# Optimization experiments

Hardware: AMD Instinct MI355X
Metric: run time of the kernel (lower is better)

Reference implementation:

```python
import jax, jax.numpy as jnp
import numpy as np

N_ITEMS = 50001   # n_items + 1 (padding row 0)
DIM = 256         # item_embedding_dim == hidden_size
PURPOSES = 3
TAU = 0.1
SEQ_LEN = 50
BATCH = 128
EPS = 0.01
STDV = 1.0 / np.sqrt(DIM)


def setup_inputs() -> dict:
    key = jax.random.key(0)
    ks = jax.random.split(key, 7)
    u = lambda k, s: jax.random.uniform(k, s, jnp.float32, -STDV, STDV)
    emb = u(ks[0], (N_ITEMS, DIM)).at[0].set(0.0)  # padding_idx=0
    emb_purpose = u(ks[1], (PURPOSES, DIM))
    w_ih = u(ks[2], (PURPOSES, 3 * DIM, DIM))
    w_hh = u(ks[3], (PURPOSES, 3 * DIM, DIM))
    b_ih = u(ks[4], (PURPOSES, 3 * DIM))
    b_hh = u(ks[5], (PURPOSES, 3 * DIM))
    seq = jax.random.randint(ks[6], (SEQ_LEN, BATCH), 0, N_ITEMS)
    return {"seq": seq, "emb": emb, "emb_purpose": emb_purpose,
            "w_ih": w_ih, "w_hh": w_hh, "b_ih": b_ih, "b_hh": b_hh}


def _psru(w_ih, w_hh, b_ih, b_hh, seq_embs, concen):
    # seq_embs: [B,S,D], concen: [B,S] -> final hidden [B,D]
    B = seq_embs.shape[0]
    H = w_hh.shape[1]

    def cell(h, xs):
        x, c = xs  # x: [B,D], c: [B]
        gi = x @ w_ih.T + b_ih
        gh = h @ w_hh.T + b_hh
        i_r, i_i, i_n = jnp.split(gi, 3, axis=1)
        h_r, h_i, h_n = jnp.split(gh, 3, axis=1)
        resetgate = jax.nn.sigmoid(i_r + h_r)
        inputgate = jax.nn.sigmoid(i_i + h_i)
        newgate = jnp.tanh(i_n + resetgate * h_n)
        cf = jnp.where(c >= EPS, c, 0.0)[:, None]  # concen gating
        hy = h - cf * inputgate * (h - newgate)
        return hy, None

    h0 = jnp.zeros((B, H), seq_embs.dtype)
    hN, _ = jax.lax.scan(cell, h0, (jnp.swapaxes(seq_embs, 0, 1), concen.T))
    return hN


def reference(seq, emb, emb_purpose, w_ih, w_hh, b_ih, b_hh):
    s = seq.T                               # [B,S]
    mask = (s != 0).astype(emb.dtype)       # padding mask
    seq_embs = emb[s]                       # [B,S,D]
    concen_score = jnp.einsum('bsd,pd->bsp', seq_embs, emb_purpose)
    concen_w = jax.nn.softmax(concen_score / TAU, axis=2) * mask[:, :, None]
    # run one PSRU per purpose, batched with vmap over the purpose axis
    hn = jax.vmap(_psru, in_axes=(0, 0, 0, 0, None, 2))(
        w_ih, w_hh, b_ih, b_hh, seq_embs, concen_w)   # [P,B,D]
    # target = arange(n_items) -> pos_embs = full embedding table
    tcw = jax.nn.softmax(emb @ emb_purpose.T, axis=1)  # [T,P]
    # scores[b,t] = sum_p tcw[t,p] * <hn[p,b,:], emb[t,:]>
    scores = jnp.einsum('pbd,td,tp->bt', hn, emb, tcw)  # [B,T]
    return scores
```

## Files before the change

kernel.cpp:

```cpp
#include <hip/hip_runtime.h>
#include <hip/hip_bf16.h>

#define S_LEN 50
#define BATCH 128
#define DIM 256
#define NITEMS 50001
#define NPAD 50048
#define GDIM 768
#define NSEQ 6400

typedef __attribute__((ext_vector_type(8))) short short8;
typedef __attribute__((ext_vector_type(4))) short short4_;
typedef __attribute__((ext_vector_type(4))) float float4_;

static __device__ __forceinline__ unsigned short f2bf(float x){
  union { float f; unsigned u; } v; v.f = x;
  unsigned r = v.u + 0x7FFFu + ((v.u >> 16) & 1u);
  return (unsigned short)(r >> 16);
}
static __device__ __forceinline__ float bf2f(unsigned short h){
  union { unsigned u; float f; } v; v.u = ((unsigned)h) << 16;
  return v.f;
}
static __device__ __forceinline__ float rcpf_(float x){ return __builtin_amdgcn_rcpf(x); }
static __device__ __forceinline__ float exp2f_(float x){ return __builtin_amdgcn_exp2f(x); }

__global__ __launch_bounds__(256) void k_prep(
        const float* __restrict__ wih, const float* __restrict__ whh,
        unsigned short* __restrict__ wihT, unsigned short* __restrict__ whh_bf,
        const float* __restrict__ emb, const float* __restrict__ embp,
        unsigned short* __restrict__ embT, float* __restrict__ tcw,
        const int* __restrict__ seq, unsigned short* __restrict__ xT,
        float* __restrict__ cfb){
  __shared__ unsigned short sT[8192];
  int bid = blockIdx.x;
  int tid = threadIdx.x;
  if (bid < 576){
    int i = bid*256 + tid;
    float4_ y = ((const float4_*)whh)[i];
    short4_ v;
    #pragma unroll
    for (int j=0;j<4;j++) v[j] = (short)f2bf(y[j]);
    ((short4_*)whh_bf)[i] = v;
    return;
  }
  int w = tid >> 6, lane = tid & 63;
  int r16 = w*4 + (lane >> 4);
  int c0  = lane & 15;
  if (bid < 720){
    int bx = bid - 576;
    const float4_* er = (const float4_*)(wih + (size_t)(bx*16 + r16)*DIM);
    #pragma unroll
    for (int k=0;k<4;k++){
      float4_ v = er[k*16 + c0];
      short4_ o;
      #pragma unroll
      for (int jj=0;jj<4;jj++) o[jj] = (short)f2bf(v[jj]);
      int di = k*64 + c0*4;
      int kf = di >> 5, qd = (di >> 3) & 3, j = di & 7;
      *(short4_*)(sT + (kf*64 + r16 + qd*16)*8 + j) = o;
    }
    __syncthreads();
    unsigned short* dst = wihT + (size_t)bx*4096 + tid*16;
    *(short8*)(dst)     = *(const short8*)(sT + tid*16);
    *(short8*)(dst + 8) = *(const short8*)(sT + tid*16 + 8);
    return;
  }
  if (bid < 3848){
    int bx = bid - 720;
    int row = bx*16 + r16;
    bool valid = row < NITEMS;
    const float4_* er = (const float4_*)(emb + (size_t)row*DIM);
    const float4_* pp = (const float4_*)embp;
    float d0=0.f, d1=0.f, d2=0.f;
    #pragma unroll
    for (int k=0;k<4;k++){
      float4_ v = valid ? er[k*16 + c0] : float4_{0.f,0.f,0.f,0.f};
      short4_ o;
      #pragma unroll
      for (int jj=0;jj<4;jj++) o[jj] = (short)f2bf(v[jj]);
      int di = k*64 + c0*4;
      int kf = di >> 5, qd = (di >> 3) & 3, j = di & 7;
      *(short4_*)(sT + (kf*64 + r16 + qd*16)*8 + j) = o;
      float4_ e0 = pp[k*16 + c0], e1 = pp[64 + k*16 + c0], e2 = pp[128 + k*16 + c0];
      #pragma unroll
      for (int jj=0;jj<4;jj++){ d0 += v[jj]*e0[jj]; d1 += v[jj]*e1[jj]; d2 += v[jj]*e2[jj]; }
    }
    #pragma unroll
    for (int off=1; off<16; off<<=1){
      d0 += __shfl_xor(d0,off); d1 += __shfl_xor(d1,off); d2 += __shfl_xor(d2,off);
    }
    if (c0 == 0 && valid){
      float m = fmaxf(d0, fmaxf(d1,d2));
      float a0 = __expf(d0-m), a1 = __expf(d1-m), a2 = __expf(d2-m);
      float inv = rcpf_(a0+a1+a2);
      tcw[row*3+0] = a0*inv; tcw[row*3+1] = a1*inv; tcw[row*3+2] = a2*inv;
    }
    __syncthreads();
    unsigned short* dst = embT + (size_t)bx*4096 + tid*16;
    *(short8*)(dst)     = *(const short8*)(sT + tid*16);
    *(short8*)(dst + 8) = *(const short8*)(sT + tid*16 + 8);
    return;
  }
  {
    int bx = bid - 3848;
    int wid = bx*16 + r16;
    int s = wid >> 7, b = wid & 127;
    int item = seq[s*BATCH + b];
    const float4_* er = (const float4_*)(emb + (size_t)item*DIM);
    const float4_* pp = (const float4_*)embp;
    float d0=0.f, d1=0.f, d2=0.f;
    #pragma unroll
    for (int k=0;k<4;k++){
      float4_ v = er[k*16 + c0];
      short4_ o;
      #pragma unroll
      for (int jj=0;jj<4;jj++) o[jj] = (short)f2bf(v[jj]);
      int di = k*64 + c0*4;
      int kf = di >> 5, qd = (di >> 3) & 3, j = di & 7;
      *(short4_*)(sT + (kf*64 + r16 + qd*16)*8 + j) = o;
      float4_ e0 = pp[k*16 + c0], e1 = pp[64 + k*16 + c0], e2 = pp[128 + k*16 + c0];
      #pragma unroll
      for (int jj=0;jj<4;jj++){ d0 += v[jj]*e0[jj]; d1 += v[jj]*e1[jj]; d2 += v[jj]*e2[jj]; }
    }
    #pragma unroll
    for (int off=1; off<16; off<<=1){
      d0 += __shfl_xor(d0,off); d1 += __shfl_xor(d1,off); d2 += __shfl_xor(d2,off);
    }
    if (c0 == 0){
      float m = fmaxf(d0, fmaxf(d1,d2));
      float a0 = __expf((d0-m)*10.f), a1 = __expf((d1-m)*10.f), a2 = __expf((d2-m)*10.f);
      float inv = (item != 0) ? rcpf_(a0+a1+a2) : 0.f;
      float cc0 = a0*inv, cc1 = a1*inv, cc2 = a2*inv;
      cfb[wid]          = (cc0 >= 0.01f) ? cc0 : 0.f;
      cfb[NSEQ + wid]   = (cc1 >= 0.01f) ? cc1 : 0.f;
      cfb[2*NSEQ + wid] = (cc2 >= 0.01f) ? cc2 : 0.f;
    }
    __syncthreads();
    unsigned short* dst = xT + (size_t)bx*4096 + tid*16;
    *(short8*)(dst)     = *(const short8*)(sT + tid*16);
    *(short8*)(dst + 8) = *(const short8*)(sT + tid*16 + 8);
  }
}

__global__ __launch_bounds__(256) void k_gi(const unsigned short* __restrict__ xT,
        const unsigned short* __restrict__ wihT, const float* __restrict__ bih,
        const float* __restrict__ bhh, unsigned short* __restrict__ gi2){
  int p  = blockIdx.z;
  int wv = threadIdx.x >> 6;
  int lane = threadIdx.x & 63;
  int col = lane & 15, q = lane >> 4;
  int mt = blockIdx.y*4 + wv;
  float4_ z4 = {0.f,0.f,0.f,0.f};
  float4_ acc[4];
  #pragma unroll
  for (int t=0;t<4;t++) acc[t] = z4;
  #pragma unroll
  for (int kf=0; kf<8; kf++){
    short8 a = *(const short8*)(xT + (((size_t)mt*8 + kf)*64 + lane)*8);
    #pragma unroll
    for (int t=0;t<4;t++){
      short8 bb = *(const short8*)(wihT + (((size_t)(p*48 + blockIdx.x*4 + t)*8 + kf)*64 + lane)*8);
      acc[t] = __builtin_amdgcn_mfma_f32_16x16x32_bf16(a, bb, acc[t], 0, 0, 0);
    }
  }
  int s     = blockIdx.y >> 1;
  int slice = (blockIdx.y & 1)*4 + wv;
  size_t X = (size_t)(p*S_LEN + s)*8 + slice;
  int g = blockIdx.x >> 2;
  #pragma unroll
  for (int t=0;t<4;t++){
    int nn = blockIdx.x*4 + t;
    int wc = (nn >> 1) & 7;
    int tt = nn & 1;
    int n  = nn*16 + col;
    float bv = bih[p*GDIM + n] + ((g < 2) ? bhh[p*GDIM + n] : 0.f);
    short4_ ov;
    #pragma unroll
    for (int i=0;i<4;i++) ov[i] = (short)f2bf(acc[t][i] + bv);
    *(short4_*)(gi2 + X*12288 + (size_t)(g*16 + wc*2 + tt)*256 + lane*4) = ov;
  }
}

__global__ __launch_bounds__(512) __attribute__((amdgpu_waves_per_eu(2, 2)))
void k_rnn(const unsigned short* __restrict__ whh_bf,
         const unsigned short* __restrict__ gi2, const float* __restrict__ bhh,
         const float* __restrict__ cfb, unsigned short* __restrict__ hnT){
  extern __shared__ char lds[];
  float* cfs = (float*)(lds + 147456);
  int p  = blockIdx.x >> 3;
  int slice = blockIdx.x & 7;
  int b0 = slice * 16;
  int tid = threadIdx.x;
  int w = tid >> 6, lane = tid & 63;
  int col = lane & 15;
  int q = lane >> 4;
  int kq = q * 8;
  const unsigned short* Wp = whh_bf + (size_t)p*GDIM*DIM;

  for (int i = tid; i < 8192; i += 512) ((unsigned short*)lds)[i] = 0;
  for (int i = tid; i < 800; i += 512) cfs[i] = cfb[p*NSEQ + (i>>4)*BATCH + b0 + (i&15)];
  {
    const unsigned short* Wn = Wp + (size_t)512*DIM;
    #pragma unroll
    for (int r = 0; r < 16; r++){
      int j = r*512 + tid;
      int kf = j >> 10, row = (j >> 2) & 255, qs = j & 3;
      short8 v = *(const short8*)(Wn + (size_t)row*DIM + kf*32 + ((qs ^ ((row>>1)&3)) << 3));
      *(short8*)(lds + 16384 + j*16) = v;
    }
  }

  float bias_n0 = bhh[p*GDIM + 512 + w*32 + col];
  float bias_n1 = bhh[p*GDIM + 512 + w*32 + 16 + col];

  short8 Bf[8][4];
  #pragma unroll
  for (int kf=0; kf<8; kf++){
    #pragma unroll
    for (int t=0;t<4;t++){
      int gc = (t>>1)*256 + w*32 + (t&1)*16 + col;
      Bf[kf][t] = *(const short8*)(Wp + ((size_t)gc << 8) + kf*32 + kq);
      asm volatile("" : "+a"(Bf[kf][t]));
    }
  }
  const char* wn0 = lds + 16384 + (size_t)(w*32 + col)*64 + ((q ^ ((col>>1)&3)) << 4);
  const char* wn1 = wn0 + 16*64;
  int swz  = (lane & 7) << 4;
  float hreg[2][4];
  #pragma unroll
  for (int t=0;t<2;t++){
    #pragma unroll
    for (int i=0;i<4;i++) hreg[t][i] = 0.f;
  }
  const size_t GSTRIDE = (size_t)8*12288;
  const unsigned short* gbase =
      gi2 + ((size_t)p*S_LEN*8 + slice)*12288 + (size_t)(w*2)*256 + lane*4;
  short4_ cur[6], nxt[6];
  #pragma unroll
  for (int t=0;t<6;t++)
    cur[t] = *(const short4_*)(gbase + (t>>1)*4096 + (t&1)*256);
  __syncthreads();

  const float K1 = -1.442695041f;
  const float K2 =  2.885390082f;
  float4_ z4 = {0.f,0.f,0.f,0.f};
  for (int s = 0; s < S_LEN; s++){
    int rbuf = s & 1, wbuf = rbuf ^ 1;
    int sn = (s+1 < S_LEN) ? s+1 : 0;
    const unsigned short* gnp = gbase + (size_t)sn*GSTRIDE;
    #pragma unroll
    for (int t=0;t<6;t++)
      nxt[t] = *(const short4_*)(gnp + (t>>1)*4096 + (t&1)*256);
    float4_ acc[6];
    #pragma unroll
    for (int t=0;t<6;t++) acc[t] = z4;
    const char* hrow = lds + rbuf*8192 + col*512;
    #pragma unroll
    for (int kf=0; kf<8; kf++){
      int ko = (kf*64 + q*16);
      short8 a = *(const short8*)(hrow + (ko ^ swz));
      #pragma unroll
      for (int t=0;t<4;t++)
        acc[t] = __builtin_amdgcn_mfma_f32_16x16x32_bf16(a, Bf[kf][t], acc[t], 0, 0, 0);
      short8 b4 = *(const short8*)(wn0 + kf*16384);
      acc[4] = __builtin_amdgcn_mfma_f32_16x16x32_bf16(a, b4, acc[4], 0, 0, 0);
      short8 b5 = *(const short8*)(wn1 + kf*16384);
      acc[5] = __builtin_amdgcn_mfma_f32_16x16x32_bf16(a, b5, acc[5], 0, 0, 0);
    }
    float4_ cfv = *(const float4_*)(cfs + s*16 + 4*q);
    char* wbase = lds + wbuf*8192;
    int d0b = 2*(w*32 + col);
    #pragma unroll
    for (int i=0;i<4;i++){
      int rb = 4*q + i;
      float hy01[2];
      #pragma unroll
      for (int t=0;t<2;t++){
        float bn = t ? bias_n1 : bias_n0;
        float r = rcpf_(1.f + exp2f_(K1*(bf2f((unsigned short)cur[t][i])   + acc[t][i])));
        float z = rcpf_(1.f + exp2f_(K1*(bf2f((unsigned short)cur[2+t][i]) + acc[2+t][i])));
        float pre = bf2f((unsigned short)cur[4+t][i]) + r*(acc[4+t][i] + bn);
        float n = 1.f - 2.f*rcpf_(exp2f_(K2*pre) + 1.f);
        float ho = hreg[t][i];
        float hy = ho - cfv[i]*z*(ho - n);
        hreg[t][i] = hy;
        hy01[t] = hy;
      }
      unsigned pk;
      asm("v_cvt_pk_bf16_f32 %0, %1, %2" : "=v"(pk) : "v"(hy01[0]), "v"(hy01[1]));
      char* rowp = wbase + rb*512;
      int sw = (rb & 7) << 4;
      *(unsigned short*)(rowp + (d0b ^ sw))        = (unsigned short)pk;
      *(unsigned short*)(rowp + ((d0b + 32) ^ sw)) = (unsigned short)(pk >> 16);
    }
    #pragma unroll
    for (int t=0;t<6;t++) cur[t] = nxt[t];
    __syncthreads();
  }
  #pragma unroll
  for (int t=0; t<2; t++){
    int d  = w*32 + t*16 + col;
    int kf = d >> 5;
    int qd = (d >> 3) & 3;
    int j  = d & 7;
    #pragma unroll
    for (int i=0; i<4; i++){
      int rb = 4*q + i;
      hnT[(((size_t)p*8 + slice)*8 + kf)*512 + (size_t)(rb + qd*16)*8 + j] = f2bf(hreg[t][i]);
    }
  }
}

__global__ __launch_bounds__(256) void k_score(const unsigned short* __restrict__ embT,
        const unsigned short* __restrict__ hnT, const float* __restrict__ tcw,
        float* __restrict__ out){
  __shared__ float sm[64*129];
  int w = threadIdx.x >> 6, lane = threadIdx.x & 63;
  int col = lane & 15, q = lane >> 4;
  int t16 = blockIdx.x*4 + w;
  int trow = t16*16 + col;
  float4_ z4 = {0.f,0.f,0.f,0.f};
  float4_ acc[3][8];
  #pragma unroll
  for (int p=0;p<3;p++){
    #pragma unroll
    for (int m=0;m<8;m++) acc[p][m] = z4;
  }
  #pragma unroll
  for (int kf=0; kf<8; kf++){
    short8 bb = *(const short8*)(embT + (((size_t)t16*8 + kf)*64 + lane)*8);
    #pragma unroll
    for (int p=0;p<3;p++){
      #pragma unroll
      for (int m=0;m<8;m++){
        short8 a = *(const short8*)(hnT + ((((size_t)p*8 + m)*8 + kf)*512) + lane*8);
        acc[p][m] = __builtin_amdgcn_mfma_f32_16x16x32_bf16(a, bb, acc[p][m], 0, 0, 0);
      }
    }
  }
  float w0=0.f, w1=0.f, w2=0.f;
  if (trow < NITEMS){ w0 = tcw[trow*3+0]; w1 = tcw[trow*3+1]; w2 = tcw[trow*3+2]; }
  #pragma unroll
  for (int m=0;m<8;m++){
    #pragma unroll
    for (int i=0;i<4;i++){
      sm[(w*16 + col)*129 + m*16 + 4*q + i] =
          w0*acc[0][m][i] + w1*acc[1][m][i] + w2*acc[2][m][i];
    }
  }
  __syncthreads();
  int trowW = blockIdx.x*64 + lane;
  if (trowW < NITEMS){
    float* orow = out + trowW;
    #pragma unroll 4
    for (int c=0; c<32; c++){
      int b = w*32 + c;
      orow[(size_t)b*NITEMS] = sm[lane*129 + b];
    }
  }
}

extern "C" void kernel_launch(void* const* d_in, const int* in_sizes, int n_in,
                              void* d_out, int out_size, void* d_ws, size_t ws_size,
                              hipStream_t stream) {
  const int*   seq  = (const int*)d_in[0];
  const float* emb  = (const float*)d_in[1];
  const float* embp = (const float*)d_in[2];
  const float* wih  = (const float*)d_in[3];
  const float* whh  = (const float*)d_in[4];
  const float* bih  = (const float*)d_in[5];
  const float* bhh  = (const float*)d_in[6];
  float* out = (float*)d_out;

  char* ws = (char*)d_ws;
  size_t off = 0;
  auto alloc = [&](size_t bytes) -> void* {
    void* r = ws + off; off += (bytes + 255) & ~(size_t)255; return r;
  };
  unsigned short* embT   = (unsigned short*)alloc((size_t)NPAD*DIM*2);
  unsigned short* xT     = (unsigned short*)alloc((size_t)NSEQ*DIM*2);
  unsigned short* wihT   = (unsigned short*)alloc((size_t)3*GDIM*DIM*2);
  unsigned short* whh_bf = (unsigned short*)alloc((size_t)3*GDIM*DIM*2);
  unsigned short* gi2    = (unsigned short*)alloc((size_t)3*NSEQ*GDIM*2);
  float* tcw = (float*)alloc((size_t)NITEMS*3*4);
  float* cfb = (float*)alloc((size_t)3*NSEQ*4);
  unsigned short* hnT = (unsigned short*)alloc((size_t)3*BATCH*DIM*2);

  k_prep<<<4248, 256, 0, stream>>>(wih, whh, wihT, whh_bf,
                                   emb, embp, embT, tcw, seq, xT, cfb);
  dim3 gg(GDIM/64, NSEQ/64, 3);
  k_gi<<<gg, 256, 0, stream>>>(xT, wihT, bih, bhh, gi2);

  (void)hipFuncSetAttribute((const void*)k_rnn,
        hipFuncAttributeMaxDynamicSharedMemorySize, 150656);
  k_rnn<<<24, 512, 150656, stream>>>(whh_bf, gi2, bhh, cfb, hnT);

  k_score<<<NPAD/64, 256, 0, stream>>>(embT, hnT, tcw, out);
}
```

Before: 190.7 us.

## Overlap embedding-table conversion with the serial RNN kernel via extra blocks

The bf16 conversion of the full embedding table, along with the per-item purpose softmax (tcw), moves out of the prep kernel. It now runs in extra blocks of the recurrent kernel, alongside the 24 latency-bound RNN blocks, so this bandwidth-heavy work can hide behind the serial recurrence. The W_hh bf16 conversion moves into the k_gi launch as trailing blocks, which shrinks the prep kernel. The risk is that the extra blocks inherit the large dynamic LDS allocation and therefore run at low occupancy. They could also contend with the RNN blocks for memory bandwidth or CUs.

Result: faster. 182.8 us (-4.1%).

```diff
diff --git a/kernel.cpp b/kernel.cpp
--- a/kernel.cpp
+++ b/kernel.cpp
@@ -26,30 +26,18 @@
 static __device__ __forceinline__ float exp2f_(float x){ return __builtin_amdgcn_exp2f(x); }
 
 __global__ __launch_bounds__(256) void k_prep(
-        const float* __restrict__ wih, const float* __restrict__ whh,
-        unsigned short* __restrict__ wihT, unsigned short* __restrict__ whh_bf,
+        const float* __restrict__ wih, unsigned short* __restrict__ wihT,
         const float* __restrict__ emb, const float* __restrict__ embp,
-        unsigned short* __restrict__ embT, float* __restrict__ tcw,
         const int* __restrict__ seq, unsigned short* __restrict__ xT,
         float* __restrict__ cfb){
   __shared__ unsigned short sT[8192];
   int bid = blockIdx.x;
   int tid = threadIdx.x;
-  if (bid < 576){
-    int i = bid*256 + tid;
-    float4_ y = ((const float4_*)whh)[i];
-    short4_ v;
-    #pragma unroll
-    for (int j=0;j<4;j++) v[j] = (short)f2bf(y[j]);
-    ((short4_*)whh_bf)[i] = v;
-    return;
-  }
   int w = tid >> 6, lane = tid & 63;
   int r16 = w*4 + (lane >> 4);
   int c0  = lane & 15;
-  if (bid < 720){
-    int bx = bid - 576;
-    const float4_* er = (const float4_*)(wih + (size_t)(bx*16 + r16)*DIM);
+  if (bid < 144){
+    const float4_* er = (const float4_*)(wih + (size_t)(bid*16 + r16)*DIM);
     #pragma unroll
     for (int k=0;k<4;k++){
       float4_ v = er[k*16 + c0];
@@ -61,49 +49,13 @@
       *(short4_*)(sT + (kf*64 + r16 + qd*16)*8 + j) = o;
     }
     __syncthreads();
-    unsigned short* dst = wihT + (size_t)bx*4096 + tid*16;
+    unsigned short* dst = wihT + (size_t)bid*4096 + tid*16;
     *(short8*)(dst)     = *(const short8*)(sT + tid*16);
     *(short8*)(dst + 8) = *(const short8*)(sT + tid*16 + 8);
     return;
   }
-  if (bid < 3848){
-    int bx = bid - 720;
-    int row = bx*16 + r16;
-    bool valid = row < NITEMS;
-    const float4_* er = (const float4_*)(emb + (size_t)row*DIM);
-    const float4_* pp = (const float4_*)embp;
-    float d0=0.f, d1=0.f, d2=0.f;
-    #pragma unroll
-    for (int k=0;k<4;k++){
-      float4_ v = valid ? er[k*16 + c0] : float4_{0.f,0.f,0.f,0.f};
-      short4_ o;
-      #pragma unroll
-      for (int jj=0;jj<4;jj++) o[jj] = (short)f2bf(v[jj]);
-      int di = k*64 + c0*4;
-      int kf = di >> 5, qd = (di >> 3) & 3, j = di & 7;
-      *(short4_*)(sT + (kf*64 + r16 + qd*16)*8 + j) = o;
-      float4_ e0 = pp[k*16 + c0], e1 = pp[64 + k*16 + c0], e2 = pp[128 + k*16 + c0];
-      #pragma unroll
-      for (int jj=0;jj<4;jj++){ d0 += v[jj]*e0[jj]; d1 += v[jj]*e1[jj]; d2 += v[jj]*e2[jj]; }
-    }
-    #pragma unroll
-    for (int off=1; off<16; off<<=1){
-      d0 += __shfl_xor(d0,off); d1 += __shfl_xor(d1,off); d2 += __shfl_xor(d2,off);
-    }
-    if (c0 == 0 && valid){
-      float m = fmaxf(d0, fmaxf(d1,d2));
-      float a0 = __expf(d0-m), a1 = __expf(d1-m), a2 = __expf(d2-m);
-      float inv = rcpf_(a0+a1+a2);
-      tcw[row*3+0] = a0*inv; tcw[row*3+1] = a1*inv; tcw[row*3+2] = a2*inv;
-    }
-    __syncthreads();
-    unsigned short* dst = embT + (size_t)bx*4096 + tid*16;
-    *(short8*)(dst)     = *(const short8*)(sT + tid*16);
-    *(short8*)(dst + 8) = *(const short8*)(sT + tid*16 + 8);
-    return;
-  }
   {
-    int bx = bid - 3848;
+    int bx = bid - 144;
     int wid = bx*16 + r16;
     int s = wid >> 7, b = wid & 127;
     int item = seq[s*BATCH + b];
@@ -145,12 +97,27 @@
 
 __global__ __launch_bounds__(256) void k_gi(const unsigned short* __restrict__ xT,
         const unsigned short* __restrict__ wihT, const float* __restrict__ bih,
-        const float* __restrict__ bhh, unsigned short* __restrict__ gi2){
-  int p  = blockIdx.z;
-  int wv = threadIdx.x >> 6;
-  int lane = threadIdx.x & 63;
+        const float* __restrict__ bhh, unsigned short* __restrict__ gi2,
+        const float* __restrict__ whh, unsigned short* __restrict__ whh_bf){
+  int bid = blockIdx.x;
+  int tid = threadIdx.x;
+  if (bid >= 3600){
+    int i = (bid - 3600)*256 + tid;
+    float4_ y = ((const float4_*)whh)[i];
+    short4_ v;
+    #pragma unroll
+    for (int j=0;j<4;j++) v[j] = (short)f2bf(y[j]);
+    ((short4_*)whh_bf)[i] = v;
+    return;
+  }
+  int nx  = bid % 12;
+  int rem = bid / 12;
+  int yy  = rem % 100;
+  int p   = rem / 100;
+  int wv = tid >> 6;
+  int lane = tid & 63;
   int col = lane & 15, q = lane >> 4;
-  int mt = blockIdx.y*4 + wv;
+  int mt = yy*4 + wv;
   float4_ z4 = {0.f,0.f,0.f,0.f};
   float4_ acc[4];
   #pragma unroll
@@ -160,17 +127,17 @@
     short8 a = *(const short8*)(xT + (((size_t)mt*8 + kf)*64 + lane)*8);
     #pragma unroll
     for (int t=0;t<4;t++){
-      short8 bb = *(const short8*)(wihT + (((size_t)(p*48 + blockIdx.x*4 + t)*8 + kf)*64 + lane)*8);
+      short8 bb = *(const short8*)(wihT + (((size_t)(p*48 + nx*4 + t)*8 + kf)*64 + lane)*8);
       acc[t] = __builtin_amdgcn_mfma_f32_16x16x32_bf16(a, bb, acc[t], 0, 0, 0);
     }
   }
-  int s     = blockIdx.y >> 1;
-  int slice = (blockIdx.y & 1)*4 + wv;
+  int s     = yy >> 1;
+  int slice = (yy & 1)*4 + wv;
   size_t X = (size_t)(p*S_LEN + s)*8 + slice;
-  int g = blockIdx.x >> 2;
+  int g = nx >> 2;
   #pragma unroll
   for (int t=0;t<4;t++){
-    int nn = blockIdx.x*4 + t;
+    int nn = nx*4 + t;
     int wc = (nn >> 1) & 7;
     int tt = nn & 1;
     int n  = nn*16 + col;
@@ -185,13 +152,58 @@
 __global__ __launch_bounds__(512) __attribute__((amdgpu_waves_per_eu(2, 2)))
 void k_rnn(const unsigned short* __restrict__ whh_bf,
          const unsigned short* __restrict__ gi2, const float* __restrict__ bhh,
-         const float* __restrict__ cfb, unsigned short* __restrict__ hnT){
+         const float* __restrict__ cfb, unsigned short* __restrict__ hnT,
+         const float* __restrict__ emb, const float* __restrict__ embp,
+         unsigned short* __restrict__ embT, float* __restrict__ tcw){
   extern __shared__ char lds[];
+  int bid = blockIdx.x;
+  int tid = threadIdx.x;
+  if (bid >= 24){
+    int sub = tid >> 8;
+    int t2  = tid & 255;
+    unsigned short* sT = (unsigned short*)lds + sub*8192;
+    int w = t2 >> 6, lane = t2 & 63;
+    int r16 = w*4 + (lane >> 4);
+    int c0  = lane & 15;
+    int bx2 = (bid - 24)*2 + sub;
+    int row = bx2*16 + r16;
+    bool valid = row < NITEMS;
+    const float4_* er = (const float4_*)(emb + (size_t)row*DIM);
+    const float4_* pp = (const float4_*)embp;
+    float d0=0.f, d1=0.f, d2=0.f;
+    #pragma unroll
+    for (int k=0;k<4;k++){
+      float4_ v = valid ? er[k*16 + c0] : float4_{0.f,0.f,0.f,0.f};
+      short4_ o;
+      #pragma unroll
+      for (int jj=0;jj<4;jj++) o[jj] = (short)f2bf(v[jj]);
+      int di = k*64 + c0*4;
+      int kf = di >> 5, qd = (di >> 3) & 3, j = di & 7;
+      *(short4_*)(sT + (kf*64 + r16 + qd*16)*8 + j) = o;
+      float4_ e0 = pp[k*16 + c0], e1 = pp[64 + k*16 + c0], e2 = pp[128 + k*16 + c0];
+      #pragma unroll
+      for (int jj=0;jj<4;jj++){ d0 += v[jj]*e0[jj]; d1 += v[jj]*e1[jj]; d2 += v[jj]*e2[jj]; }
+    }
+    #pragma unroll
+    for (int off=1; off<16; off<<=1){
+      d0 += __shfl_xor(d0,off); d1 += __shfl_xor(d1,off); d2 += __shfl_xor(d2,off);
+    }
+    if (c0 == 0 && valid){
+      float m = fmaxf(d0, fmaxf(d1,d2));
+      float a0 = __expf(d0-m), a1 = __expf(d1-m), a2 = __expf(d2-m);
+      float inv = rcpf_(a0+a1+a2);
+      tcw[row*3+0] = a0*inv; tcw[row*3+1] = a1*inv; tcw[row*3+2] = a2*inv;
+    }
+    __syncthreads();
+    unsigned short* dst = embT + (size_t)bx2*4096 + t2*16;
+    *(short8*)(dst)     = *(const short8*)(sT + t2*16);
+    *(short8*)(dst + 8) = *(const short8*)(sT + t2*16 + 8);
+    return;
+  }
   float* cfs = (float*)(lds + 147456);
-  int p  = blockIdx.x >> 3;
-  int slice = blockIdx.x & 7;
+  int p  = bid >> 3;
+  int slice = bid & 7;
   int b0 = slice * 16;
-  int tid = threadIdx.x;
   int w = tid >> 6, lane = tid & 63;
   int col = lane & 15;
   int q = lane >> 4;
@@ -387,14 +399,13 @@
   float* cfb = (float*)alloc((size_t)3*NSEQ*4);
   unsigned short* hnT = (unsigned short*)alloc((size_t)3*BATCH*DIM*2);
 
-  k_prep<<<4248, 256, 0, stream>>>(wih, whh, wihT, whh_bf,
-                                   emb, embp, embT, tcw, seq, xT, cfb);
-  dim3 gg(GDIM/64, NSEQ/64, 3);
-  k_gi<<<gg, 256, 0, stream>>>(xT, wihT, bih, bhh, gi2);
+  k_prep<<<544, 256, 0, stream>>>(wih, wihT, emb, embp, seq, xT, cfb);
+  k_gi<<<4176, 256, 0, stream>>>(xT, wihT, bih, bhh, gi2, whh, whh_bf);
 
   (void)hipFuncSetAttribute((const void*)k_rnn,
         hipFuncAttributeMaxDynamicSharedMemorySize, 150656);
-  k_rnn<<<24, 512, 150656, stream>>>(whh_bf, gi2, bhh, cfb, hnT);
+  k_rnn<<<1588, 512, 150656, stream>>>(whh_bf, gi2, bhh, cfb, hnT,
+                                       emb, embp, embT, tcw);
 
   k_score<<<NPAD/64, 256, 0, stream>>>(embT, hnT, tcw, out);
 }
```
